# Performance work log

Measured on AMD Instinct MI355X. Metric: run time of the kernel, lower is better.

The kernel has to match this reference:

```python
import jax, jax.numpy as jnp
import numpy as np

N = 100000          # num nodes
E_C = 6_400_000     # connection edges
E_D = 400_000       # destination edges
F_IN = 5
H = 8
BN_EPS = 1e-5
L2_EPS = 1e-12


def setup_inputs() -> dict:
    key = jax.random.key(0)
    ks = jax.random.split(key, 16)
    d = {}
    d["x"] = jax.random.normal(ks[0], (N, F_IN), dtype=jnp.float32)
    d["edge_index_connections"] = jax.random.randint(ks[1], (2, E_C), 0, N, dtype=jnp.int64)
    d["edge_index_destinations"] = jax.random.randint(ks[2], (2, E_D), 0, N, dtype=jnp.int64)
    # SAGEConv weights: lin_l (neighbor aggregate), lin_r (root), no bias
    d["W1l"] = jax.random.normal(ks[3], (H, F_IN), jnp.float32) * 0.3
    d["W1r"] = jax.random.normal(ks[4], (H, F_IN), jnp.float32) * 0.3
    d["W2l"] = jax.random.normal(ks[5], (H, H), jnp.float32) * 0.3
    d["W2r"] = jax.random.normal(ks[6], (H, H), jnp.float32) * 0.3
    d["W3l"] = jax.random.normal(ks[7], (H, H), jnp.float32) * 0.3
    d["W3r"] = jax.random.normal(ks[8], (H, H), jnp.float32) * 0.3
    d["W4l"] = jax.random.normal(ks[9], (H, H), jnp.float32) * 0.3
    d["W4r"] = jax.random.normal(ks[10], (H, H), jnp.float32) * 0.3
    # LazyBatchNorm1d affine params (init gamma=1, beta=0)
    for i in range(1, 5):
        d[f"g{i}"] = jnp.ones((H,), jnp.float32)
        d[f"b{i}"] = jnp.zeros((H,), jnp.float32)
    return d


def _sage(x, ei, Wl, Wr):
    # PyG SAGEConv(mean aggr, normalize=True, bias=False):
    # out = lin_l(mean_{j in N(i)} x_j) + lin_r(x_i); then L2 normalize rows.
    src, dst = ei[0], ei[1]
    msgs = x[src]                                            # [E, F] gather
    s = jax.ops.segment_sum(msgs, dst, num_segments=N)       # [N, F]
    cnt = jax.ops.segment_sum(jnp.ones((ei.shape[1],), x.dtype), dst, num_segments=N)
    mean = s / jnp.maximum(cnt, 1.0)[:, None]                # zero for isolated nodes
    out = mean @ Wl.T + x @ Wr.T                             # [N, H]
    nrm = jnp.linalg.norm(out, axis=-1, keepdims=True)
    return out / jnp.maximum(nrm, L2_EPS)


def _bn(x, g, b):
    # BatchNorm1d in training mode: per-feature batch stats (biased variance)
    m = x.mean(axis=0)
    v = x.var(axis=0)
    return (x - m) * jax.lax.rsqrt(v + BN_EPS) * g + b


def reference(x, edge_index_connections, edge_index_destinations,
              W1l, W1r, W2l, W2r, W3l, W3r, W4l, W4r,
              g1, b1, g2, b2, g3, b3, g4, b4):
    eic = edge_index_connections
    eid = edge_index_destinations
    h = _bn(jax.nn.relu(_sage(x, eic, W1l, W1r)), g1, b1)
    # ITERATIONS_BEFORE_DESTINATION = 1 (conv4 + bn2)
    h = _bn(jax.nn.relu(_sage(h, eic, W4l, W4r)), g2, b2)
    # destination pass (conv2 + bn3)
    h = _bn(jax.nn.relu(_sage(h, eid, W2l, W2r)), g3, b3)
    # ITERATIONS_AFTER_DESTINATION = 2 (conv3 + bn4)
    for _ in range(2):
        h = _bn(jax.nn.relu(_sage(h, eic, W3l, W3r)), g4, b4)
    return h
```

## Files before the change

kernel.cpp:

```cpp
#include <hip/hip_runtime.h>

#define NN 100000
#define EC 6400000
#define ED 400000
#define BN_EPS 1e-5f
#define NSB ((NN + 255) >> 8)
#define NCH 256
#define CSR_CAP 19200
#define CHUNK_OF(E) (((((E) + NCH - 1) / NCH) + 3) & ~3)


__global__ __launch_bounds__(1024)
void hist_pass(const int* __restrict__ ei, int E, int* __restrict__ bhist) {
    __shared__ int h[NSB];
    for (int i = threadIdx.x; i < NSB; i += 1024) h[i] = 0;
    __syncthreads();
    int k = blockIdx.x;
    int chunk = CHUNK_OF(E);
    int beg = k * chunk, end = min(E, beg + chunk);
    for (int e = beg + threadIdx.x * 4; e < end; e += 1024 * 4) {
        int4 d4 = *(const int4*)&ei[E + e];
        atomicAdd(&h[d4.x >> 8], 1);
        atomicAdd(&h[d4.y >> 8], 1);
        atomicAdd(&h[d4.z >> 8], 1);
        atomicAdd(&h[d4.w >> 8], 1);
    }
    __syncthreads();
    for (int i = threadIdx.x; i < NSB; i += 1024) bhist[i * NCH + k] = h[i];
}

__global__ __launch_bounds__(256)
void row_scan(int* __restrict__ bhist, int* __restrict__ total) {
    int b = blockIdx.x;
    int* row = bhist + b * NCH;
    __shared__ int wsum[4];
    int lane = threadIdx.x & 63, w = threadIdx.x >> 6;
    int v = row[threadIdx.x];
    int x = v;
    #pragma unroll
    for (int sh = 1; sh < 64; sh <<= 1) { int y = __shfl_up(x, sh); if (lane >= sh) x += y; }
    if (lane == 63) wsum[w] = x;
    __syncthreads();
    int wb = 0;
    #pragma unroll
    for (int j = 0; j < 4; ++j) if (j < w) wb += wsum[j];
    row[threadIdx.x] = wb + x - v;
    if (threadIdx.x == 255) total[b] = wb + x;
}

__global__ void bucket_base(const int* __restrict__ total, int* __restrict__ bbase) {
    __shared__ int wsum[4];
    __shared__ int carry;
    if (threadIdx.x == 0) carry = 0;
    __syncthreads();
    int lane = threadIdx.x & 63, w = threadIdx.x >> 6;
    for (int s = 0; s < NSB; s += 256) {
        int idx = s + threadIdx.x;
        int v = (idx < NSB) ? total[idx] : 0;
        int x = v;
        #pragma unroll
        for (int sh = 1; sh < 64; sh <<= 1) { int y = __shfl_up(x, sh); if (lane >= sh) x += y; }
        if (lane == 63) wsum[w] = x;
        __syncthreads();
        int wb = 0;
        #pragma unroll
        for (int j = 0; j < 4; ++j) if (j < w) wb += wsum[j];
        int all = wsum[0] + wsum[1] + wsum[2] + wsum[3];
        if (idx < NSB) bbase[idx] = carry + wb + x - v;
        __syncthreads();
        if (threadIdx.x == 0) carry += all;
        __syncthreads();
    }
}

__global__ __launch_bounds__(1024)
void scatter_pairs(const int* __restrict__ ei, int E,
                   const int* __restrict__ bhist, const int* __restrict__ bbase,
                   unsigned* __restrict__ packed) {
    __shared__ int cur[NSB];
    int k = blockIdx.x;
    for (int b = threadIdx.x; b < NSB; b += 1024)
        cur[b] = bbase[b] + bhist[b * NCH + k];
    __syncthreads();
    int chunk = CHUNK_OF(E);
    int beg = k * chunk, end = min(E, beg + chunk);
    for (int e = beg + threadIdx.x * 4; e < end; e += 1024 * 4) {
        int4 s4 = *(const int4*)&ei[e];
        int4 d4 = *(const int4*)&ei[E + e];
        { int p = atomicAdd(&cur[d4.x >> 8], 1); packed[p] = (unsigned)s4.x | ((unsigned)(d4.x & 255) << 17); }
        { int p = atomicAdd(&cur[d4.y >> 8], 1); packed[p] = (unsigned)s4.y | ((unsigned)(d4.y & 255) << 17); }
        { int p = atomicAdd(&cur[d4.z >> 8], 1); packed[p] = (unsigned)s4.z | ((unsigned)(d4.z & 255) << 17); }
        { int p = atomicAdd(&cur[d4.w >> 8], 1); packed[p] = (unsigned)s4.w | ((unsigned)(d4.w & 255) << 17); }
    }
}

__global__ __launch_bounds__(256)
void sb_csr(const unsigned* __restrict__ packed,
            const int* __restrict__ bbase, const int* __restrict__ total,
            int* __restrict__ csr, int* __restrict__ offs, int* __restrict__ deg,
            float* __restrict__ inv) {
    __shared__ int h[256];
    __shared__ int loff[256];
    __shared__ int ws2[4];
    __shared__ int ebuf[CSR_CAP];
    int b = blockIdx.x;
    int ebeg = bbase[b], ecnt = total[b];
    int node0 = b << 8;
    int nn = min(256, NN - node0);
    h[threadIdx.x] = 0;
    __syncthreads();
    for (int e = threadIdx.x; e < ecnt; e += 256)
        atomicAdd(&h[packed[ebeg + e] >> 17], 1);
    __syncthreads();
    {
        int lane = threadIdx.x & 63, w = threadIdx.x >> 6;
        int v = h[threadIdx.x], x = v;
        #pragma unroll
        for (int sh = 1; sh < 64; sh <<= 1) { int y = __shfl_up(x, sh); if (lane >= sh) x += y; }
        if (lane == 63) ws2[w] = x;
        __syncthreads();
        int wb = 0;
        #pragma unroll
        for (int j = 0; j < 4; ++j) if (j < w) wb += ws2[j];
        int excl = wb + x - v;
        loff[threadIdx.x] = excl;
        if (threadIdx.x < nn) {
            int node = node0 + threadIdx.x;
            offs[node] = ebeg + excl;
            deg[node]  = v;
            inv[node]  = 1.0f / (float)(v > 1 ? v : 1);
        }
    }
    __syncthreads();
    if (ecnt <= CSR_CAP) {
        for (int e = threadIdx.x; e < ecnt; e += 256) {
            unsigned u = packed[ebeg + e];
            int p = atomicAdd(&loff[u >> 17], 1);
            ebuf[p] = (int)(u & 0x1FFFF);
        }
        __syncthreads();
        for (int e = threadIdx.x; e < ecnt; e += 256) csr[ebeg + e] = ebuf[e];
    } else {
        for (int e = threadIdx.x; e < ecnt; e += 256) {
            unsigned u = packed[ebeg + e];
            int p = atomicAdd(&loff[u >> 17], 1);
            csr[ebeg + p] = (int)(u & 0x1FFFF);
        }
    }
}

__global__ __launch_bounds__(256)
void prep_misc(const float* __restrict__ x, const float* __restrict__ W1l,
               const float* __restrict__ W1r, float* __restrict__ xp,
               float* __restrict__ W1lp, float* __restrict__ W1rp) {
    int t = blockIdx.x * 256 + threadIdx.x;
    if (t < 64) {
        int f = t >> 3, k = t & 7;
        W1lp[t] = (k < 5) ? W1l[f * 5 + k] : 0.f;
        W1rp[t] = (k < 5) ? W1r[f * 5 + k] : 0.f;
    }
    for (int idx = t; idx < NN * 8; idx += gridDim.x * 256) {
        int f = idx & 7, i = idx >> 3;
        xp[idx] = (f < 5) ? x[i * 5 + f] : 0.f;
    }
}

template<bool APPLY_BN>
__global__ __launch_bounds__(256)
void sage_layer8(const float* __restrict__ hin,
                 const float* __restrict__ stats_in,
                 const float* __restrict__ gin, const float* __restrict__ bin,
                 const int* __restrict__ offs, const int* __restrict__ deg,
                 const int* __restrict__ csr, const float* __restrict__ inv,
                 const float* __restrict__ Wl, const float* __restrict__ Wr,
                 float* __restrict__ hout, float* __restrict__ stats_out) {
    __shared__ float bl[16];
    int tid = threadIdx.x;
    if (tid < 16) bl[tid] = 0.f;
    __syncthreads();
    int wave = tid >> 6, lane = tid & 63, g = lane >> 3, f = lane & 7;

    float sc[8], sh[8];
    #pragma unroll
    for (int k = 0; k < 8; ++k) { sc[k] = 1.f; sh[k] = 0.f; }
    if constexpr (APPLY_BN) {
        #pragma unroll
        for (int k = 0; k < 8; ++k) {
            float m = stats_in[k * 16] * (1.f / NN);
            float v = stats_in[(8 + k) * 16] * (1.f / NN) - m * m;
            float is = rsqrtf(v + BN_EPS);
            sc[k] = gin[k] * is;
            sh[k] = bin[k] - m * sc[k];
        }
    }
    float wl[8], wr[8];
    #pragma unroll
    for (int k = 0; k < 8; ++k) { wl[k] = Wl[f * 8 + k]; wr[k] = Wr[f * 8 + k]; }

    float acc_r = 0.f, acc_r2 = 0.f;
    const int stride = gridDim.x * 32;
    for (int i0 = (blockIdx.x * 4 + wave) * 8; i0 < NN; i0 += stride) {
        int i = i0 + g;
        int ic = min(i, NN - 1);
        bool ok = (i < NN);
        int d = ok ? deg[ic] : 0;
        int o = offs[ic];
        float a0 = 0, a1 = 0, a2 = 0, a3 = 0, a4 = 0, a5 = 0, a6 = 0, a7 = 0;
        for (int b = 0; b < d; b += 8) {
            int e = b + f;
            int cv = csr[o + e];
            float m = (e < d) ? 1.f : 0.f;
            unsigned s = min((unsigned)cv & 0x1FFFFu, (unsigned)(NN - 1));
            const float4* rp = (const float4*)(hin + (size_t)s * 8);
            float4 r0 = rp[0];
            float4 r1 = rp[1];
            a0 = fmaf(r0.x, m, a0); a1 = fmaf(r0.y, m, a1);
            a2 = fmaf(r0.z, m, a2); a3 = fmaf(r0.w, m, a3);
            a4 = fmaf(r1.x, m, a4); a5 = fmaf(r1.y, m, a5);
            a6 = fmaf(r1.z, m, a6); a7 = fmaf(r1.w, m, a7);
        }
        #pragma unroll
        for (int msk = 1; msk < 8; msk <<= 1) {
            a0 += __shfl_xor(a0, msk); a1 += __shfl_xor(a1, msk);
            a2 += __shfl_xor(a2, msk); a3 += __shfl_xor(a3, msk);
            a4 += __shfl_xor(a4, msk); a5 += __shfl_xor(a5, msk);
            a6 += __shfl_xor(a6, msk); a7 += __shfl_xor(a7, msk);
        }
        float im = inv[ic];
        float dnz = (d > 0) ? 1.f : 0.f;
        const float4* hp = (const float4*)(hin + (size_t)ic * 8);
        float4 h0 = hp[0];
        float4 h1 = hp[1];
        float hk[8] = { h0.x, h0.y, h0.z, h0.w, h1.x, h1.y, h1.z, h1.w };
        float ac[8] = { a0, a1, a2, a3, a4, a5, a6, a7 };
        float y = 0.f;
        #pragma unroll
        for (int k = 0; k < 8; ++k) {
            float mk = fmaf(sc[k], ac[k] * im, sh[k] * dnz);
            float hh = fmaf(sc[k], hk[k], sh[k]);
            y = fmaf(mk, wl[k], y);
            y = fmaf(hh, wr[k], y);
        }
        float n2 = y * y;
        n2 += __shfl_xor(n2, 1);
        n2 += __shfl_xor(n2, 2);
        n2 += __shfl_xor(n2, 4);
        float z = y / fmaxf(sqrtf(n2), 1e-12f);
        float r = fmaxf(z, 0.f);
        r = ok ? r : 0.f;
        if (ok) hout[(size_t)i * 8 + f] = r;
        acc_r += r;
        acc_r2 += r * r;
    }
    atomicAdd(&bl[f], acc_r);
    atomicAdd(&bl[8 + f], acc_r2);
    __syncthreads();
    if (tid < 16) atomicAdd(&stats_out[tid * 16], bl[tid]);
}

__global__ void apply_bn_out(const float* __restrict__ hin,
                             const float* __restrict__ stats,
                             const float* __restrict__ g, const float* __restrict__ b,
                             float* __restrict__ out) {
    int t = blockIdx.x * blockDim.x + threadIdx.x;
    if (t >= NN * 8) return;
    int f = t & 7;
    float m = stats[f * 16] * (1.0f / NN);
    float v = stats[(8 + f) * 16] * (1.0f / NN) - m * m;
    float sc = g[f] * rsqrtf(v + BN_EPS);
    float sh = b[f] - m * sc;
    out[t] = fmaf(hin[t], sc, sh);
}


static inline char* bump(char*& p, size_t bytes) {
    char* r = p;
    p += (bytes + 255) & ~(size_t)255;
    return r;
}

extern "C" void kernel_launch(void* const* d_in, const int* in_sizes, int n_in,
                              void* d_out, int out_size, void* d_ws, size_t ws_size,
                              hipStream_t stream) {
    const float* x   = (const float*)d_in[0];
    const int* eic   = (const int*)d_in[1];
    const int* eid   = (const int*)d_in[2];
    const float* W1l = (const float*)d_in[3];
    const float* W1r = (const float*)d_in[4];
    const float* W2l = (const float*)d_in[5];
    const float* W2r = (const float*)d_in[6];
    const float* W3l = (const float*)d_in[7];
    const float* W3r = (const float*)d_in[8];
    const float* W4l = (const float*)d_in[9];
    const float* W4r = (const float*)d_in[10];
    const float* g1 = (const float*)d_in[11];
    const float* b1 = (const float*)d_in[12];
    const float* g2 = (const float*)d_in[13];
    const float* b2 = (const float*)d_in[14];
    const float* g3 = (const float*)d_in[15];
    const float* b3 = (const float*)d_in[16];
    const float* g4 = (const float*)d_in[17];
    const float* b4 = (const float*)d_in[18];
    float* out = (float*)d_out;

    char* p = (char*)d_ws;
    float* stats   = (float*)bump(p, 5 * 256 * 4);
    size_t zero_bytes = (size_t)(p - (char*)d_ws);
    int*   bhist_c = (int*)  bump(p, (size_t)NSB * NCH * 4);
    int*   bhist_d = (int*)  bump(p, (size_t)NSB * NCH * 4);
    int*   total_c = (int*)  bump(p, NSB * 4);
    int*   bbase_c = (int*)  bump(p, NSB * 4);
    int*   total_d = (int*)  bump(p, NSB * 4);
    int*   bbase_d = (int*)  bump(p, NSB * 4);
    int*   offs_c  = (int*)  bump(p, NN * 4);
    int*   deg_c   = (int*)  bump(p, NN * 4);
    float* inv_c   = (float*)bump(p, NN * 4);
    int*   offs_d  = (int*)  bump(p, NN * 4);
    int*   deg_d   = (int*)  bump(p, NN * 4);
    float* inv_d   = (float*)bump(p, NN * 4);
    int*   csr_c   = (int*)  bump(p, ((size_t)EC + 64) * 4);
    int*   csr_d   = (int*)  bump(p, ((size_t)ED + 64) * 4);
    float* xp32    = (float*)bump(p, (size_t)NN * 8 * 4);
    float* W1lp    = (float*)bump(p, 64 * 4);
    float* W1rp    = (float*)bump(p, 64 * 4);
    unsigned* packed_d = (unsigned*)bump(p, (size_t)ED * 4);
    char* pc = p;
    unsigned* packed_c = (unsigned*)bump(p, (size_t)EC * 4);
    char* pr = pc;
    float* r_a = (float*)bump(pr, (size_t)NN * 8 * 4);
    float* r_b = (float*)bump(pr, (size_t)NN * 8 * 4);
    (void)ws_size; (void)in_sizes; (void)n_in; (void)out_size;

    hipMemsetAsync(d_ws, 0, zero_bytes, stream);

    hist_pass<<<NCH, 1024, 0, stream>>>(eic, EC, bhist_c);
    hist_pass<<<NCH, 1024, 0, stream>>>(eid, ED, bhist_d);
    row_scan<<<NSB, 256, 0, stream>>>(bhist_c, total_c);
    row_scan<<<NSB, 256, 0, stream>>>(bhist_d, total_d);
    bucket_base<<<1, 256, 0, stream>>>(total_c, bbase_c);
    bucket_base<<<1, 256, 0, stream>>>(total_d, bbase_d);
    scatter_pairs<<<NCH, 1024, 0, stream>>>(eic, EC, bhist_c, bbase_c, packed_c);
    scatter_pairs<<<NCH, 1024, 0, stream>>>(eid, ED, bhist_d, bbase_d, packed_d);
    sb_csr<<<NSB, 256, 0, stream>>>(packed_c, bbase_c, total_c, csr_c, offs_c, deg_c, inv_c);
    sb_csr<<<NSB, 256, 0, stream>>>(packed_d, bbase_d, total_d, csr_d, offs_d, deg_d, inv_d);
    prep_misc<<<512, 256, 0, stream>>>(x, W1l, W1r, xp32, W1lp, W1rp);

    const int LB = 2048;
    sage_layer8<false><<<LB, 256, 0, stream>>>(
        xp32, nullptr, nullptr, nullptr,
        offs_c, deg_c, csr_c, inv_c, W1lp, W1rp, r_a, stats + 0);
    sage_layer8<true><<<LB, 256, 0, stream>>>(
        r_a, stats + 0, g1, b1,
        offs_c, deg_c, csr_c, inv_c, W4l, W4r, r_b, stats + 256);
    sage_layer8<true><<<LB, 256, 0, stream>>>(
        r_b, stats + 256, g2, b2,
        offs_d, deg_d, csr_d, inv_d, W2l, W2r, r_a, stats + 512);
    sage_layer8<true><<<LB, 256, 0, stream>>>(
        r_a, stats + 512, g3, b3,
        offs_c, deg_c, csr_c, inv_c, W3l, W3r, r_b, stats + 768);
    sage_layer8<true><<<LB, 256, 0, stream>>>(
        r_b, stats + 768, g4, b4,
        offs_c, deg_c, csr_c, inv_c, W3l, W3r, r_a, stats + 1024);
    apply_bn_out<<<(NN * 8 + 255) / 256, 256, 0, stream>>>(r_a, stats + 1024, g4, b4, out);
}
```

Before: 639.9 us.

## Pad CSR rows to 4 and gather four neighbors per lane with int4

The CSR build now pads each node's edge list to a multiple of four, using separate padded bucket bases. This lets the SAGE layer read neighbor indices as aligned int4 vectors, with each lane handling four neighbors per iteration. The layer kernel now launches one block per 32 nodes without a grid-stride loop, and it accumulates BN statistics with per-thread shared atomics. The aim is more memory-level parallelism in the gather and fewer index loads. The cost is a larger CSR buffer, reads of padding entries that get masked out, and more shared atomics. Padded slots are never written, so they hold leftover values, but the index clamp keeps their addresses in range.

```diff
diff --git a/kernel.cpp b/kernel.cpp
--- a/kernel.cpp
+++ b/kernel.cpp
@@ -48,27 +48,33 @@
     if (threadIdx.x == 255) total[b] = wb + x;
 }
 
-__global__ void bucket_base(const int* __restrict__ total, int* __restrict__ bbase) {
-    __shared__ int wsum[4];
-    __shared__ int carry;
-    if (threadIdx.x == 0) carry = 0;
+__global__ void bucket_base(const int* __restrict__ total,
+                            int* __restrict__ bbase, int* __restrict__ cbase) {
+    __shared__ int wsum[4], wsum2[4];
+    __shared__ int carry, carry2;
+    if (threadIdx.x == 0) { carry = 0; carry2 = 0; }
     __syncthreads();
     int lane = threadIdx.x & 63, w = threadIdx.x >> 6;
     for (int s = 0; s < NSB; s += 256) {
         int idx = s + threadIdx.x;
-        int v = (idx < NSB) ? total[idx] : 0;
-        int x = v;
-        #pragma unroll
-        for (int sh = 1; sh < 64; sh <<= 1) { int y = __shfl_up(x, sh); if (lane >= sh) x += y; }
-        if (lane == 63) wsum[w] = x;
-        __syncthreads();
-        int wb = 0;
-        #pragma unroll
-        for (int j = 0; j < 4; ++j) if (j < w) wb += wsum[j];
+        int v  = (idx < NSB) ? total[idx] : 0;
+        int v2 = (idx < NSB) ? (((total[idx] + 3) & ~3) + 1024) : 0;
+        int x = v, x2 = v2;
+        #pragma unroll
+        for (int sh = 1; sh < 64; sh <<= 1) {
+            int y = __shfl_up(x, sh);  if (lane >= sh) x += y;
+            int y2 = __shfl_up(x2, sh); if (lane >= sh) x2 += y2;
+        }
+        if (lane == 63) { wsum[w] = x; wsum2[w] = x2; }
+        __syncthreads();
+        int wb = 0, wb2 = 0;
+        #pragma unroll
+        for (int j = 0; j < 4; ++j) if (j < w) { wb += wsum[j]; wb2 += wsum2[j]; }
         int all = wsum[0] + wsum[1] + wsum[2] + wsum[3];
-        if (idx < NSB) bbase[idx] = carry + wb + x - v;
-        __syncthreads();
-        if (threadIdx.x == 0) carry += all;
+        int all2 = wsum2[0] + wsum2[1] + wsum2[2] + wsum2[3];
+        if (idx < NSB) { bbase[idx] = carry + wb + x - v; cbase[idx] = carry2 + wb2 + x2 - v2; }
+        __syncthreads();
+        if (threadIdx.x == 0) { carry += all; carry2 += all2; }
         __syncthreads();
     }
 }
@@ -97,14 +103,16 @@
 __global__ __launch_bounds__(256)
 void sb_csr(const unsigned* __restrict__ packed,
             const int* __restrict__ bbase, const int* __restrict__ total,
+            const int* __restrict__ cbase,
             int* __restrict__ csr, int* __restrict__ offs, int* __restrict__ deg,
             float* __restrict__ inv) {
     __shared__ int h[256];
     __shared__ int loff[256];
     __shared__ int ws2[4];
+    __shared__ int ptot_s;
     __shared__ int ebuf[CSR_CAP];
     int b = blockIdx.x;
-    int ebeg = bbase[b], ecnt = total[b];
+    int ebeg = bbase[b], ecnt = total[b], cbeg = cbase[b];
     int node0 = b << 8;
     int nn = min(256, NN - node0);
     h[threadIdx.x] = 0;
@@ -114,7 +122,9 @@
     __syncthreads();
     {
         int lane = threadIdx.x & 63, w = threadIdx.x >> 6;
-        int v = h[threadIdx.x], x = v;
+        int v = h[threadIdx.x];
+        int pv = (v + 3) & ~3;
+        int x = pv;
         #pragma unroll
         for (int sh = 1; sh < 64; sh <<= 1) { int y = __shfl_up(x, sh); if (lane >= sh) x += y; }
         if (lane == 63) ws2[w] = x;
@@ -122,29 +132,31 @@
         int wb = 0;
         #pragma unroll
         for (int j = 0; j < 4; ++j) if (j < w) wb += ws2[j];
-        int excl = wb + x - v;
+        int excl = wb + x - pv;
         loff[threadIdx.x] = excl;
+        if (threadIdx.x == 255) ptot_s = wb + x;
         if (threadIdx.x < nn) {
             int node = node0 + threadIdx.x;
-            offs[node] = ebeg + excl;
+            offs[node] = cbeg + excl;
             deg[node]  = v;
             inv[node]  = 1.0f / (float)(v > 1 ? v : 1);
         }
     }
     __syncthreads();
-    if (ecnt <= CSR_CAP) {
+    int ptot = ptot_s;
+    if (ptot <= CSR_CAP) {
         for (int e = threadIdx.x; e < ecnt; e += 256) {
             unsigned u = packed[ebeg + e];
             int p = atomicAdd(&loff[u >> 17], 1);
             ebuf[p] = (int)(u & 0x1FFFF);
         }
         __syncthreads();
-        for (int e = threadIdx.x; e < ecnt; e += 256) csr[ebeg + e] = ebuf[e];
+        for (int e = threadIdx.x; e < ptot; e += 256) csr[cbeg + e] = ebuf[e];
     } else {
         for (int e = threadIdx.x; e < ecnt; e += 256) {
             unsigned u = packed[ebeg + e];
             int p = atomicAdd(&loff[u >> 17], 1);
-            csr[ebeg + p] = (int)(u & 0x1FFFF);
+            csr[cbeg + p] = (int)(u & 0x1FFFF);
         }
     }
 }
@@ -197,63 +209,78 @@
     #pragma unroll
     for (int k = 0; k < 8; ++k) { wl[k] = Wl[f * 8 + k]; wr[k] = Wr[f * 8 + k]; }
 
-    float acc_r = 0.f, acc_r2 = 0.f;
-    const int stride = gridDim.x * 32;
-    for (int i0 = (blockIdx.x * 4 + wave) * 8; i0 < NN; i0 += stride) {
-        int i = i0 + g;
-        int ic = min(i, NN - 1);
-        bool ok = (i < NN);
-        int d = ok ? deg[ic] : 0;
-        int o = offs[ic];
-        float a0 = 0, a1 = 0, a2 = 0, a3 = 0, a4 = 0, a5 = 0, a6 = 0, a7 = 0;
-        for (int b = 0; b < d; b += 8) {
-            int e = b + f;
-            int cv = csr[o + e];
-            float m = (e < d) ? 1.f : 0.f;
-            unsigned s = min((unsigned)cv & 0x1FFFFu, (unsigned)(NN - 1));
-            const float4* rp = (const float4*)(hin + (size_t)s * 8);
-            float4 r0 = rp[0];
-            float4 r1 = rp[1];
-            a0 = fmaf(r0.x, m, a0); a1 = fmaf(r0.y, m, a1);
-            a2 = fmaf(r0.z, m, a2); a3 = fmaf(r0.w, m, a3);
-            a4 = fmaf(r1.x, m, a4); a5 = fmaf(r1.y, m, a5);
-            a6 = fmaf(r1.z, m, a6); a7 = fmaf(r1.w, m, a7);
-        }
-        #pragma unroll
-        for (int msk = 1; msk < 8; msk <<= 1) {
-            a0 += __shfl_xor(a0, msk); a1 += __shfl_xor(a1, msk);
-            a2 += __shfl_xor(a2, msk); a3 += __shfl_xor(a3, msk);
-            a4 += __shfl_xor(a4, msk); a5 += __shfl_xor(a5, msk);
-            a6 += __shfl_xor(a6, msk); a7 += __shfl_xor(a7, msk);
-        }
-        float im = inv[ic];
-        float dnz = (d > 0) ? 1.f : 0.f;
-        const float4* hp = (const float4*)(hin + (size_t)ic * 8);
-        float4 h0 = hp[0];
-        float4 h1 = hp[1];
-        float hk[8] = { h0.x, h0.y, h0.z, h0.w, h1.x, h1.y, h1.z, h1.w };
-        float ac[8] = { a0, a1, a2, a3, a4, a5, a6, a7 };
-        float y = 0.f;
-        #pragma unroll
-        for (int k = 0; k < 8; ++k) {
-            float mk = fmaf(sc[k], ac[k] * im, sh[k] * dnz);
-            float hh = fmaf(sc[k], hk[k], sh[k]);
-            y = fmaf(mk, wl[k], y);
-            y = fmaf(hh, wr[k], y);
-        }
-        float n2 = y * y;
-        n2 += __shfl_xor(n2, 1);
-        n2 += __shfl_xor(n2, 2);
-        n2 += __shfl_xor(n2, 4);
-        float z = y / fmaxf(sqrtf(n2), 1e-12f);
-        float r = fmaxf(z, 0.f);
-        r = ok ? r : 0.f;
-        if (ok) hout[(size_t)i * 8 + f] = r;
-        acc_r += r;
-        acc_r2 += r * r;
-    }
-    atomicAdd(&bl[f], acc_r);
-    atomicAdd(&bl[8 + f], acc_r2);
+    int i = (blockIdx.x * 4 + wave) * 8 + g;
+    int d = deg[i];
+    int o = offs[i];
+    const int e0 = f * 4;
+    float a0 = 0, a1 = 0, a2 = 0, a3 = 0, a4 = 0, a5 = 0, a6 = 0, a7 = 0;
+    for (int b = 0; b < d; b += 32) {
+        int base = b + e0;
+        int4 c4 = *(const int4*)(csr + o + base);
+        unsigned s0 = min((unsigned)c4.x & 0x1FFFFu, (unsigned)(NN - 1));
+        unsigned s1 = min((unsigned)c4.y & 0x1FFFFu, (unsigned)(NN - 1));
+        unsigned s2 = min((unsigned)c4.z & 0x1FFFFu, (unsigned)(NN - 1));
+        unsigned s3 = min((unsigned)c4.w & 0x1FFFFu, (unsigned)(NN - 1));
+        const float4* p0 = (const float4*)(hin + (size_t)s0 * 8);
+        const float4* p1 = (const float4*)(hin + (size_t)s1 * 8);
+        const float4* p2 = (const float4*)(hin + (size_t)s2 * 8);
+        const float4* p3 = (const float4*)(hin + (size_t)s3 * 8);
+        float4 r00 = p0[0], r01 = p0[1];
+        float4 r10 = p1[0], r11 = p1[1];
+        float4 r20 = p2[0], r21 = p2[1];
+        float4 r30 = p3[0], r31 = p3[1];
+        float m0 = (base + 0 < d) ? 1.f : 0.f;
+        float m1 = (base + 1 < d) ? 1.f : 0.f;
+        float m2 = (base + 2 < d) ? 1.f : 0.f;
+        float m3 = (base + 3 < d) ? 1.f : 0.f;
+        a0 = fmaf(r00.x, m0, a0); a1 = fmaf(r00.y, m0, a1);
+        a2 = fmaf(r00.z, m0, a2); a3 = fmaf(r00.w, m0, a3);
+        a4 = fmaf(r01.x, m0, a4); a5 = fmaf(r01.y, m0, a5);
+        a6 = fmaf(r01.z, m0, a6); a7 = fmaf(r01.w, m0, a7);
+        a0 = fmaf(r10.x, m1, a0); a1 = fmaf(r10.y, m1, a1);
+        a2 = fmaf(r10.z, m1, a2); a3 = fmaf(r10.w, m1, a3);
+        a4 = fmaf(r11.x, m1, a4); a5 = fmaf(r11.y, m1, a5);
+        a6 = fmaf(r11.z, m1, a6); a7 = fmaf(r11.w, m1, a7);
+        a0 = fmaf(r20.x, m2, a0); a1 = fmaf(r20.y, m2, a1);
+        a2 = fmaf(r20.z, m2, a2); a3 = fmaf(r20.w, m2, a3);
+        a4 = fmaf(r21.x, m2, a4); a5 = fmaf(r21.y, m2, a5);
+        a6 = fmaf(r21.z, m2, a6); a7 = fmaf(r21.w, m2, a7);
+        a0 = fmaf(r30.x, m3, a0); a1 = fmaf(r30.y, m3, a1);
+        a2 = fmaf(r30.z, m3, a2); a3 = fmaf(r30.w, m3, a3);
+        a4 = fmaf(r31.x, m3, a4); a5 = fmaf(r31.y, m3, a5);
+        a6 = fmaf(r31.z, m3, a6); a7 = fmaf(r31.w, m3, a7);
+    }
+    #pragma unroll
+    for (int msk = 1; msk < 8; msk <<= 1) {
+        a0 += __shfl_xor(a0, msk); a1 += __shfl_xor(a1, msk);
+        a2 += __shfl_xor(a2, msk); a3 += __shfl_xor(a3, msk);
+        a4 += __shfl_xor(a4, msk); a5 += __shfl_xor(a5, msk);
+        a6 += __shfl_xor(a6, msk); a7 += __shfl_xor(a7, msk);
+    }
+    float im = inv[i];
+    float dnz = (d > 0) ? 1.f : 0.f;
+    const float4* hp = (const float4*)(hin + (size_t)i * 8);
+    float4 h0 = hp[0];
+    float4 h1 = hp[1];
+    float hk[8] = { h0.x, h0.y, h0.z, h0.w, h1.x, h1.y, h1.z, h1.w };
+    float ac[8] = { a0, a1, a2, a3, a4, a5, a6, a7 };
+    float y = 0.f;
+    #pragma unroll
+    for (int k = 0; k < 8; ++k) {
+        float mk = fmaf(sc[k], ac[k] * im, sh[k] * dnz);
+        float hh = fmaf(sc[k], hk[k], sh[k]);
+        y = fmaf(mk, wl[k], y);
+        y = fmaf(hh, wr[k], y);
+    }
+    float n2 = y * y;
+    n2 += __shfl_xor(n2, 1);
+    n2 += __shfl_xor(n2, 2);
+    n2 += __shfl_xor(n2, 4);
+    float z = y / fmaxf(sqrtf(n2), 1e-12f);
+    float r = fmaxf(z, 0.f);
+    hout[(size_t)i * 8 + f] = r;
+    atomicAdd(&bl[f], r);
+    atomicAdd(&bl[8 + f], r * r);
     __syncthreads();
     if (tid < 16) atomicAdd(&stats_out[tid * 16], bl[tid]);
 }
@@ -303,6 +330,8 @@
     const float* b4 = (const float*)d_in[18];
     float* out = (float*)d_out;
 
+    const size_t CPAD = (size_t)NSB * 1024 + 2048;
+
     char* p = (char*)d_ws;
     float* stats   = (float*)bump(p, 5 * 256 * 4);
     size_t zero_bytes = (size_t)(p - (char*)d_ws);
@@ -310,16 +339,18 @@
     int*   bhist_d = (int*)  bump(p, (size_t)NSB * NCH * 4);
     int*   total_c = (int*)  bump(p, NSB * 4);
     int*   bbase_c = (int*)  bump(p, NSB * 4);
+    int*   cbase_c = (int*)  bump(p, NSB * 4);
     int*   total_d = (int*)  bump(p, NSB * 4);
     int*   bbase_d = (int*)  bump(p, NSB * 4);
+    int*   cbase_d = (int*)  bump(p, NSB * 4);
     int*   offs_c  = (int*)  bump(p, NN * 4);
     int*   deg_c   = (int*)  bump(p, NN * 4);
     float* inv_c   = (float*)bump(p, NN * 4);
     int*   offs_d  = (int*)  bump(p, NN * 4);
     int*   deg_d   = (int*)  bump(p, NN * 4);
     float* inv_d   = (float*)bump(p, NN * 4);
-    int*   csr_c   = (int*)  bump(p, ((size_t)EC + 64) * 4);
-    int*   csr_d   = (int*)  bump(p, ((size_t)ED + 64) * 4);
+    int*   csr_c   = (int*)  bump(p, ((size_t)EC + CPAD) * 4);
+    int*   csr_d   = (int*)  bump(p, ((size_t)ED + CPAD) * 4);
     float* xp32    = (float*)bump(p, (size_t)NN * 8 * 4);
     float* W1lp    = (float*)bump(p, 64 * 4);
     float* W1rp    = (float*)bump(p, 64 * 4);
@@ -337,15 +368,15 @@
     hist_pass<<<NCH, 1024, 0, stream>>>(eid, ED, bhist_d);
     row_scan<<<NSB, 256, 0, stream>>>(bhist_c, total_c);
     row_scan<<<NSB, 256, 0, stream>>>(bhist_d, total_d);
-    bucket_base<<<1, 256, 0, stream>>>(total_c, bbase_c);
-    bucket_base<<<1, 256, 0, stream>>>(total_d, bbase_d);
+    bucket_base<<<1, 256, 0, stream>>>(total_c, bbase_c, cbase_c);
+    bucket_base<<<1, 256, 0, stream>>>(total_d, bbase_d, cbase_d);
     scatter_pairs<<<NCH, 1024, 0, stream>>>(eic, EC, bhist_c, bbase_c, packed_c);
     scatter_pairs<<<NCH, 1024, 0, stream>>>(eid, ED, bhist_d, bbase_d, packed_d);
-    sb_csr<<<NSB, 256, 0, stream>>>(packed_c, bbase_c, total_c, csr_c, offs_c, deg_c, inv_c);
-    sb_csr<<<NSB, 256, 0, stream>>>(packed_d, bbase_d, total_d, csr_d, offs_d, deg_d, inv_d);
+    sb_csr<<<NSB, 256, 0, stream>>>(packed_c, bbase_c, total_c, cbase_c, csr_c, offs_c, deg_c, inv_c);
+    sb_csr<<<NSB, 256, 0, stream>>>(packed_d, bbase_d, total_d, cbase_d, csr_d, offs_d, deg_d, inv_d);
     prep_misc<<<512, 256, 0, stream>>>(x, W1l, W1r, xp32, W1lp, W1rp);
 
-    const int LB = 2048;
+    const int LB = (NN + 31) / 32;
     sage_layer8<false><<<LB, 256, 0, stream>>>(
         xp32, nullptr, nullptr, nullptr,
         offs_c, deg_c, csr_c, inv_c, W1lp, W1rp, r_a, stats + 0);
```

After: 691.9 us. 8.1% more time.
